# Optimization experiments

Hardware: AMD Instinct MI355X
Metric: run time of the kernel (lower is better)

The kernel has to match this reference:

```python
import jax, jax.numpy as jnp
import numpy as np

HIDDEN = 768
FF = 3072
N_HEADS = 12
HEAD = HIDDEN // N_HEADS
WIDTH = 512  # attention window (number of attended keys, causal)
B, S = 2, 4096
EPS = 1e-6


def _rotary_sincos(seq_len, dim):
    # GPT-J style: freqs per pair, each value repeated twice (interleaved)
    inv_freq = 1.0 / (10000.0 ** (np.arange(0, dim, 2, dtype=np.float32) / dim))
    t = np.arange(seq_len, dtype=np.float32)
    ang = np.einsum('s,d->sd', t, inv_freq)              # [S, dim/2]
    ang = np.repeat(ang, 2, axis=-1)                     # [S, dim]
    return jnp.asarray(np.sin(ang))[:, None, :], jnp.asarray(np.cos(ang))[:, None, :]


def setup_inputs() -> dict:
    key = jax.random.key(0)
    ks = jax.random.split(key, 4)
    x = jax.random.normal(ks[0], (B, S, HIDDEN), dtype=jnp.float32)
    sin, cos = _rotary_sincos(S, HEAD)                   # [S,1,HEAD] each
    W_in = jax.random.normal(ks[1], (HIDDEN, 3 * HIDDEN + FF), dtype=jnp.float32) / np.sqrt(HIDDEN)
    b_in = jnp.zeros((3 * HIDDEN + FF,), dtype=jnp.float32)
    W_out = jax.random.normal(ks[2], (HIDDEN + FF, HIDDEN), dtype=jnp.float32) / np.sqrt(HIDDEN + FF)
    b_out = jnp.zeros((HIDDEN,), dtype=jnp.float32)
    w_norm = jnp.ones((HIDDEN,), dtype=jnp.float32)
    return {"x": x, "sin": sin, "cos": cos, "w_norm": w_norm,
            "W_in": W_in, "b_in": b_in, "W_out": W_out, "b_out": b_out}


def _rotate_every_two(x):
    x1 = x[..., ::2]
    x2 = x[..., 1::2]
    return jnp.stack((-x2, x1), axis=-1).reshape(x.shape)


def _apply_rope(x, sin, cos):
    # x: [B,S,H,hd]; sin/cos: [S,1,hd] -> broadcast as [1,S,1,hd]
    sin = sin[None]
    cos = cos[None]
    return x * cos + _rotate_every_two(x) * sin


def _windowed_attention(q, k, v, width):
    # q,k,v: [B,S,H,hd]; causal local attention: key j valid iff 0 <= i-j < width
    b, s, h, d = q.shape
    wb = width  # block size == window; each query block attends blocks (b-1, b)
    nb = s // wb
    scale = 1.0 / np.sqrt(d)
    qb = q.reshape(b, nb, wb, h, d)
    kp = jnp.pad(k, ((0, 0), (wb, 0), (0, 0), (0, 0))).reshape(b, nb + 1, wb, h, d)
    vp = jnp.pad(v, ((0, 0), (wb, 0), (0, 0), (0, 0))).reshape(b, nb + 1, wb, h, d)
    kb = jnp.concatenate([kp[:, :-1], kp[:, 1:]], axis=2)   # [B,nb,2wb,H,hd]
    vb = jnp.concatenate([vp[:, :-1], vp[:, 1:]], axis=2)
    scores = jnp.einsum('bnqhd,bnkhd->bnhqk', qb, kb) * scale
    qi = jnp.arange(wb)
    ki = jnp.arange(2 * wb)
    bi = jnp.arange(nb)
    diff = wb + qi[:, None] - ki[None, :]                    # i - j per block
    base = (diff >= 0) & (diff < width)                      # [wb, 2wb]
    valid_j = (bi[:, None, None] >= 1) | (ki[None, None, :] >= wb)  # j >= 0
    mask = base[None] & valid_j                              # [nb, wb, 2wb]
    neg = jnp.finfo(scores.dtype).min
    scores = jnp.where(mask[None, :, None], scores, neg)
    p = jax.nn.softmax(scores, axis=-1)
    out = jnp.einsum('bnhqk,bnkhd->bnqhd', p, vb)
    return out.reshape(b, s, h * d)


def reference(x, sin, cos, w_norm, W_in, b_in, W_out, b_out):
    # RMSNorm
    ms = jnp.mean(x * x, axis=-1, keepdims=True)
    xn = x * jax.lax.rsqrt(ms + EPS) * w_norm
    # fused QKV + FF projection
    t = xn @ W_in + b_in                                     # [B,S,3*HIDDEN+FF]
    ff = t[:, :, -FF:]
    qkv = t[:, :, :-FF].reshape(x.shape[0], x.shape[1], 3, N_HEADS, HEAD)
    q = _apply_rope(qkv[:, :, 0], sin, cos)
    k = _apply_rope(qkv[:, :, 1], sin, cos)
    v = qkv[:, :, 2]
    attn = _windowed_attention(q, k, v, WIDTH)               # [B,S,HIDDEN]
    ff = jax.nn.gelu(ff, approximate=False)
    combined = jnp.concatenate((attn, ff), axis=-1)          # [B,S,HIDDEN+FF]
    return combined @ W_out + b_out
```

## Files before the change

kernel.cpp:

```cpp
#include <hip/hip_runtime.h>
#include <hip/hip_bf16.h>

typedef short bf16x8 __attribute__((ext_vector_type(8)));
typedef float f32x4 __attribute__((ext_vector_type(4)));

#define LOG2E 1.4426950408889634f
#define QKV_E ((size_t)24*4096*64)

__device__ __forceinline__ float bfu2f(unsigned short u) {
  unsigned v = ((unsigned)u) << 16;
  return __builtin_bit_cast(float, v);
}
__device__ __forceinline__ unsigned short f2bfu(float f) {
  unsigned u = __builtin_bit_cast(unsigned, f);
  u += 0x7fffu + ((u >> 16) & 1u);
  return (unsigned short)(u >> 16);
}
__device__ __forceinline__ unsigned packbf2(float lo, float hi) {
  return (unsigned)f2bfu(lo) | ((unsigned)f2bfu(hi) << 16);
}
__device__ __forceinline__ float gelu_f(float v) {
  float a = fabsf(v) * 0.70710678118654752f;
  float t = 1.0f / (1.0f + 0.3275911f * a);
  float poly = ((((1.061405429f * t - 1.453152027f) * t + 1.421413741f) * t
                 - 0.284496736f) * t + 0.254829592f) * t;
  float erfa = 1.0f - poly * __expf(-a * a);
  float erfv = v >= 0.0f ? erfa : -erfa;
  return 0.5f * v * (1.0f + erfv);
}
__device__ __forceinline__ void gl_lds16(const ushort* g, ushort* l) {
  __builtin_amdgcn_global_load_lds(
      (const __attribute__((address_space(1))) unsigned int*)(const void*)g,
      (__attribute__((address_space(3))) unsigned int*)(void*)l, 16, 0, 0);
}
#define WAIT_VM8  asm volatile("s_waitcnt vmcnt(8)" ::: "memory")
#define WAIT_VM0  asm volatile("s_waitcnt vmcnt(0)" ::: "memory")
#define WAIT_LGKM asm volatile("s_waitcnt lgkmcnt(0)" ::: "memory")
#define BAR       __builtin_amdgcn_s_barrier()

__global__ __launch_bounds__(256) void rmsnorm_k(const float* __restrict__ x,
    const float* __restrict__ w, ushort* __restrict__ xn) {
  int row = blockIdx.x, t = threadIdx.x;
  const float* xr = x + (size_t)row * 768;
  float v0 = xr[t], v1 = xr[t + 256], v2 = xr[t + 512];
  float ss = v0 * v0 + v1 * v1 + v2 * v2;
#pragma unroll
  for (int m = 32; m >= 1; m >>= 1) ss += __shfl_xor(ss, m, 64);
  __shared__ float part[4];
  if ((t & 63) == 0) part[t >> 6] = ss;
  __syncthreads();
  float tot = part[0] + part[1] + part[2] + part[3];
  float rr = rsqrtf(tot * (1.0f / 768.0f) + 1e-6f);
  ushort* xo = xn + (size_t)row * 768;
  xo[t]       = f2bfu(v0 * rr * w[t]);
  xo[t + 256] = f2bfu(v1 * rr * w[t + 256]);
  xo[t + 512] = f2bfu(v2 * rr * w[t + 512]);
}

__global__ __launch_bounds__(256) void tcvt_k(const float* __restrict__ in,
    ushort* __restrict__ out, int R, int C) {
  __shared__ float tile[32][33];
  int c0 = blockIdx.x * 32, r0 = blockIdx.y * 32;
  int t = threadIdx.x;
  int j = t & 31, i0 = t >> 5;
#pragma unroll
  for (int i = i0; i < 32; i += 8) tile[i][j] = in[(size_t)(r0 + i) * C + c0 + j];
  __syncthreads();
#pragma unroll
  for (int i = i0; i < 32; i += 8) out[(size_t)(c0 + i) * R + r0 + j] = f2bfu(tile[j][i]);
}

__global__ __launch_bounds__(256, 4) void gemm1_k(const ushort* __restrict__ A,
    const ushort* __restrict__ Bt, const float* __restrict__ bias,
    const float* __restrict__ sn, const float* __restrict__ cs,
    ushort* __restrict__ qbuf, ushort* __restrict__ kbuf,
    ushort* __restrict__ vt, ushort* __restrict__ comb) {
  __shared__ __align__(16) ushort lds[2][128 * 64];
  const int t = threadIdx.x, lane = t & 63, w = t >> 6;
  const int wr = w >> 1, wc = w & 1;
  int bid = blockIdx.x;
  int xcd = bid & 7, local = bid >> 3;
  int grp = local / 48, r6 = local % 48;
  int bx = grp * 6 + r6 % 6;
  int by = xcd * 8 + r6 / 6;
  const int mBase = by * 128, nBase = bx * 128;

  size_t gA[4], gB[4];
  int ldst[4];
#pragma unroll
  for (int j = 0; j < 4; ++j) {
    int row = w * 32 + j * 8 + (lane >> 3);
    int gc = ((lane & 7) ^ (lane >> 3)) * 8;
    gA[j] = (size_t)(mBase + row) * 768 + gc;
    gB[j] = (size_t)(nBase + row) * 768 + gc;
    ldst[j] = (w * 32 + j * 8) * 64;
  }

  f32x4 acc[4][4];
  f32x4 z = {0.f, 0.f, 0.f, 0.f};
#pragma unroll
  for (int m = 0; m < 4; ++m)
#pragma unroll
    for (int nn = 0; nn < 4; ++nn) acc[m][nn] = z;

#pragma unroll 1
  for (int kt = 0; kt < 12; ++kt) {
    const int k0 = kt * 64;
    __syncthreads();
#pragma unroll
    for (int j = 0; j < 4; ++j) {
      gl_lds16(A + gA[j] + k0, &lds[0][0] + ldst[j]);
      gl_lds16(Bt + gB[j] + k0, &lds[1][0] + ldst[j]);
    }
    __syncthreads();
#pragma unroll
    for (int kk = 0; kk < 2; ++kk) {
      bf16x8 af[4], bff[4];
#pragma unroll
      for (int m = 0; m < 4; ++m) {
        int row = wr * 64 + m * 16 + (lane & 15);
        int slot = (kk * 4 + (lane >> 4)) ^ (lane & 7);
        af[m] = *(const bf16x8*)(&lds[0][0] + row * 64 + slot * 8);
      }
#pragma unroll
      for (int nn = 0; nn < 4; ++nn) {
        int row = wc * 64 + nn * 16 + (lane & 15);
        int slot = (kk * 4 + (lane >> 4)) ^ (lane & 7);
        bff[nn] = *(const bf16x8*)(&lds[1][0] + row * 64 + slot * 8);
      }
#pragma unroll
      for (int m = 0; m < 4; ++m)
#pragma unroll
        for (int nn = 0; nn < 4; ++nn)
          acc[m][nn] = __builtin_amdgcn_mfma_f32_16x16x32_bf16(bff[nn], af[m], acc[m][nn], 0, 0, 0);
    }
  }

  const bool isff = (nBase >= 2304);
  const int region = nBase / 768;
#pragma unroll
  for (int m = 0; m < 4; ++m) {
    int row = mBase + wr * 64 + m * 16 + (lane & 15);
    int b = row >> 12, s = row & 4095;
#pragma unroll
    for (int nn = 0; nn < 4; ++nn) {
      int col = nBase + wc * 64 + nn * 16 + ((lane >> 4) << 2);
      f32x4 v = acc[m][nn] + *(const f32x4*)(bias + col);
      if (isff) {
        ushort4 o;
        o.x = f2bfu(gelu_f(v[0]));
        o.y = f2bfu(gelu_f(v[1]));
        o.z = f2bfu(gelu_f(v[2]));
        o.w = f2bfu(gelu_f(v[3]));
        *(ushort4*)(comb + (size_t)row * 3840 + (col - 1536)) = o;
      } else {
        int rem = col - region * 768;
        int h = rem >> 6, d0 = rem & 63;
        if (region == 2) {
          int l = s & 127;
          int pnn = l >> 4, pg = (l >> 2) & 3, pr = l & 3;
          int sp = (s & ~127) | (((pnn >> 1) * 4 + pg) * 8 + (pnn & 1) * 4 + pr);
          size_t vb = (size_t)((b * 12 + h) * 64 + d0) * 4096 + sp;
          vt[vb]          = f2bfu(v[0]);
          vt[vb + 4096]   = f2bfu(v[1]);
          vt[vb + 2*4096] = f2bfu(v[2]);
          vt[vb + 3*4096] = f2bfu(v[3]);
        } else {
          f32x4 sv = *(const f32x4*)(sn + (s << 6) + d0);
          f32x4 cv = *(const f32x4*)(cs + (s << 6) + d0);
          float o0 = v[0] * cv[0] - v[1] * sv[0];
          float o1 = v[1] * cv[0] + v[0] * sv[0];
          float o2 = v[2] * cv[2] - v[3] * sv[2];
          float o3 = v[3] * cv[2] + v[2] * sv[2];
          ushort4 o;
          if (region == 0) {
            o.x = f2bfu(o0 * 0.125f); o.y = f2bfu(o1 * 0.125f);
            o.z = f2bfu(o2 * 0.125f); o.w = f2bfu(o3 * 0.125f);
            *(ushort4*)(qbuf + ((size_t)((b * 12 + h) * 4096 + s)) * 64 + d0) = o;
          } else {
            o.x = f2bfu(o0); o.y = f2bfu(o1); o.z = f2bfu(o2); o.w = f2bfu(o3);
            *(ushort4*)(kbuf + ((size_t)((b * 12 + h) * 4096 + s)) * 64 + d0) = o;
          }
        }
      }
    }
  }
}

__global__ __launch_bounds__(256, 4) void gemm2_k(const ushort* __restrict__ A,
    const ushort* __restrict__ Bt, const float* __restrict__ bias,
    float* __restrict__ out) {
  __shared__ __align__(16) ushort lds[2][128 * 64];
  const int t = threadIdx.x, lane = t & 63, w = t >> 6;
  const int wr = w >> 1, wc = w & 1;
  int bid = blockIdx.x;
  int xcd = bid & 7, local = bid >> 3;
  int g = local / 4, r4 = local % 4;
  int bx = (g % 3) * 2 + (r4 & 1);
  int by = xcd * 8 + (g / 3) * 2 + (r4 >> 1);
  const int mBase = by * 128, nBase = bx * 128;

  size_t gA[4], gB[4];
  int ldst[4];
#pragma unroll
  for (int j = 0; j < 4; ++j) {
    int row = w * 32 + j * 8 + (lane >> 3);
    int gc = ((lane & 7) ^ (lane >> 3)) * 8;
    gA[j] = (size_t)(mBase + row) * 3840 + gc;
    gB[j] = (size_t)(nBase + row) * 3840 + gc;
    ldst[j] = (w * 32 + j * 8) * 64;
  }

  f32x4 acc[4][4];
  f32x4 z = {0.f, 0.f, 0.f, 0.f};
#pragma unroll
  for (int m = 0; m < 4; ++m)
#pragma unroll
    for (int nn = 0; nn < 4; ++nn) acc[m][nn] = z;

#pragma unroll 1
  for (int kt = 0; kt < 60; ++kt) {
    const int k0 = kt * 64;
    __syncthreads();
#pragma unroll
    for (int j = 0; j < 4; ++j) {
      gl_lds16(A + gA[j] + k0, &lds[0][0] + ldst[j]);
      gl_lds16(Bt + gB[j] + k0, &lds[1][0] + ldst[j]);
    }
    __syncthreads();
#pragma unroll
    for (int kk = 0; kk < 2; ++kk) {
      bf16x8 af[4], bff[4];
#pragma unroll
      for (int m = 0; m < 4; ++m) {
        int row = wr * 64 + m * 16 + (lane & 15);
        int slot = (kk * 4 + (lane >> 4)) ^ (lane & 7);
        af[m] = *(const bf16x8*)(&lds[0][0] + row * 64 + slot * 8);
      }
#pragma unroll
      for (int nn = 0; nn < 4; ++nn) {
        int row = wc * 64 + nn * 16 + (lane & 15);
        int slot = (kk * 4 + (lane >> 4)) ^ (lane & 7);
        bff[nn] = *(const bf16x8*)(&lds[1][0] + row * 64 + slot * 8);
      }
#pragma unroll
      for (int m = 0; m < 4; ++m)
#pragma unroll
        for (int nn = 0; nn < 4; ++nn)
          acc[m][nn] = __builtin_amdgcn_mfma_f32_16x16x32_bf16(bff[nn], af[m], acc[m][nn], 0, 0, 0);
    }
  }

#pragma unroll
  for (int m = 0; m < 4; ++m) {
    int row = mBase + wr * 64 + m * 16 + (lane & 15);
#pragma unroll
    for (int nn = 0; nn < 4; ++nn) {
      int col = nBase + wc * 64 + nn * 16 + ((lane >> 4) << 2);
      f32x4 v = acc[m][nn] + *(const f32x4*)(bias + col);
      *(f32x4*)(out + (size_t)row * 768 + col) = v;
    }
  }
}

__global__ __launch_bounds__(256, 2) void attn_k(const ushort* __restrict__ qb,
    const ushort* __restrict__ kb, const ushort* __restrict__ vt,
    ushort* __restrict__ comb) {
  __shared__ __align__(16) ushort KS[2][128 * 64];
  __shared__ __align__(16) ushort VS[2][64 * 128];
  int bid = blockIdx.x;
  int nb = (bid & 7) * 96 + (bid >> 3);
  int qt = nb & 31, bh = nb >> 5;
  const int t = threadIdx.x, lane = t & 63, w = t >> 6;
  const int g = lane >> 4, q15 = lane & 15;
  const int qlo = qt * 128;
  const size_t base = (size_t)bh * 4096 * 64;

  size_t kSrc[4], vSrc[4];
  int dstOff[4];
#pragma unroll
  for (int j = 0; j < 4; ++j) {
    int ck = (w * 4 + j) * 64 + lane;
    int key = ck >> 3, sl = ck & 7;
    kSrc[j] = (size_t)key * 64 + ((sl ^ (key & 7)) << 3);
    int dd = ck >> 4, s16 = ck & 15;
    vSrc[j] = (size_t)dd * 4096 + ((s16 ^ (dd & 15)) << 3);
    dstOff[j] = (w * 4 + j) * 512;
  }

  bf16x8 qa[2][2];
#pragma unroll
  for (int m = 0; m < 2; ++m)
#pragma unroll
    for (int kk = 0; kk < 2; ++kk) {
      int row = qlo + w * 32 + m * 16 + q15;
      qa[m][kk] = *(const bf16x8*)(qb + base + (size_t)row * 64 + kk * 32 + g * 8);
    }

  f32x4 z = {0.f, 0.f, 0.f, 0.f};
  f32x4 o[2][4];
#pragma unroll
  for (int m = 0; m < 2; ++m)
#pragma unroll
    for (int df = 0; df < 4; ++df) o[m][df] = z;
  float m_run[2] = {-1e30f, -1e30f}, l_run[2] = {0.f, 0.f};

  const int t0 = qt >= 4 ? qt - 4 : 0;
  const int nt = qt - t0 + 1;
  {
    int k0 = t0 * 128;
#pragma unroll
    for (int j = 0; j < 4; ++j) {
      gl_lds16(kb + base + (size_t)k0 * 64 + kSrc[j], &KS[0][0] + dstOff[j]);
      gl_lds16(vt + base + k0 + vSrc[j], &VS[0][0] + dstOff[j]);
    }
  }

  const int qrow0 = qlo + w * 32 + q15;
#pragma unroll 1
  for (int it = 0; it < nt; ++it) {
    const int kt = t0 + it, k0 = kt * 128, cur = it & 1;
    if (it + 1 < nt) {
      int k1 = k0 + 128;
#pragma unroll
      for (int j = 0; j < 4; ++j) {
        gl_lds16(kb + base + (size_t)k1 * 64 + kSrc[j], &KS[1 - cur][0] + dstOff[j]);
        gl_lds16(vt + base + k1 + vSrc[j], &VS[1 - cur][0] + dstOff[j]);
      }
      WAIT_VM8;
    } else {
      WAIT_VM0;
    }
    BAR;
    f32x4 s[2][8];
#pragma unroll
    for (int m = 0; m < 2; ++m)
#pragma unroll
      for (int nn = 0; nn < 8; ++nn) s[m][nn] = z;
#pragma unroll
    for (int kk = 0; kk < 2; ++kk) {
      bf16x8 kf[8];
#pragma unroll
      for (int nn = 0; nn < 8; ++nn) {
        int row = nn * 16 + q15;
        int slot = (kk * 4 + g) ^ (q15 & 7);
        kf[nn] = *(const bf16x8*)(&KS[cur][0] + row * 64 + slot * 8);
      }
#pragma unroll
      for (int m = 0; m < 2; ++m)
#pragma unroll
        for (int nn = 0; nn < 8; ++nn)
          s[m][nn] = __builtin_amdgcn_mfma_f32_16x16x32_bf16(kf[nn], qa[m][kk], s[m][nn], 0, 0, 0);
    }
    if (kt == qt) {
#pragma unroll
      for (int m = 0; m < 2; ++m) {
        int ql = qrow0 + m * 16 - k0;
#pragma unroll
        for (int nn = 0; nn < 8; ++nn)
#pragma unroll
          for (int r = 0; r < 4; ++r)
            if (nn * 16 + g * 4 + r > ql) s[m][nn][r] = -3e38f;
      }
    } else if (kt == qt - 4) {
#pragma unroll
      for (int m = 0; m < 2; ++m) {
        int ql = qrow0 + m * 16 - k0;
#pragma unroll
        for (int nn = 0; nn < 8; ++nn)
#pragma unroll
          for (int r = 0; r < 4; ++r)
            if (ql - (nn * 16 + g * 4 + r) >= 512) s[m][nn][r] = -3e38f;
      }
    }
    float mx[2];
    bool need = false;
#pragma unroll
    for (int m = 0; m < 2; ++m) {
      float v = s[m][0][0];
#pragma unroll
      for (int nn = 0; nn < 8; ++nn)
#pragma unroll
        for (int r = 0; r < 4; ++r) v = fmaxf(v, s[m][nn][r]);
      v = fmaxf(v, __shfl_xor(v, 16, 64));
      v = fmaxf(v, __shfl_xor(v, 32, 64));
      mx[m] = v;
      need |= (v > m_run[m] + 8.f);
    }
    if (__any(need)) {
#pragma unroll
      for (int m = 0; m < 2; ++m) {
        float mn = fmaxf(m_run[m], mx[m]);
        float sc = exp2f((m_run[m] - mn) * LOG2E);
        m_run[m] = mn;
        l_run[m] *= sc;
#pragma unroll
        for (int df = 0; df < 4; ++df) o[m][df] *= sc;
      }
    }
#pragma unroll
    for (int m = 0; m < 2; ++m) {
      float mr = m_run[m];
      float ls = 0.f;
#pragma unroll
      for (int nn = 0; nn < 8; ++nn)
#pragma unroll
        for (int r = 0; r < 4; ++r) {
          float p = exp2f((s[m][nn][r] - mr) * LOG2E);
          s[m][nn][r] = p;
          ls += p;
        }
      ls += __shfl_xor(ls, 16, 64);
      ls += __shfl_xor(ls, 32, 64);
      l_run[m] += ls;
    }
#pragma unroll
    for (int kk2 = 0; kk2 < 4; ++kk2) {
      bf16x8 pa[2];
#pragma unroll
      for (int m = 0; m < 2; ++m) {
        int4 pi4;
        pi4.x = (int)packbf2(s[m][2*kk2][0],   s[m][2*kk2][1]);
        pi4.y = (int)packbf2(s[m][2*kk2][2],   s[m][2*kk2][3]);
        pi4.z = (int)packbf2(s[m][2*kk2+1][0], s[m][2*kk2+1][1]);
        pi4.w = (int)packbf2(s[m][2*kk2+1][2], s[m][2*kk2+1][3]);
        pa[m] = __builtin_bit_cast(bf16x8, pi4);
      }
#pragma unroll
      for (int df = 0; df < 4; ++df) {
        int row = df * 16 + q15;
        int slot = (kk2 * 4 + g) ^ q15;
        bf16x8 vf = *(const bf16x8*)(&VS[cur][0] + row * 128 + slot * 8);
#pragma unroll
        for (int m = 0; m < 2; ++m)
          o[m][df] = __builtin_amdgcn_mfma_f32_16x16x32_bf16(vf, pa[m], o[m][df], 0, 0, 0);
      }
    }
    WAIT_LGKM;
    BAR;
  }

  int b = bh / 12, h = bh % 12;
#pragma unroll
  for (int m = 0; m < 2; ++m) {
    float inv = 1.0f / l_run[m];
    int row = qrow0 + m * 16;
#pragma unroll
    for (int df = 0; df < 4; ++df) {
      ushort4 ov;
      ov.x = f2bfu(o[m][df][0] * inv);
      ov.y = f2bfu(o[m][df][1] * inv);
      ov.z = f2bfu(o[m][df][2] * inv);
      ov.w = f2bfu(o[m][df][3] * inv);
      *(ushort4*)(comb + (size_t)(b * 4096 + row) * 3840 + h * 64 + df * 16 + g * 4) = ov;
    }
  }
}

extern "C" void kernel_launch(void* const* d_in, const int* in_sizes, int n_in,
                              void* d_out, int out_size, void* d_ws, size_t ws_size,
                              hipStream_t stream) {
  (void)in_sizes; (void)n_in; (void)out_size; (void)ws_size;
  const float* x      = (const float*)d_in[0];
  const float* sin_t  = (const float*)d_in[1];
  const float* cos_t  = (const float*)d_in[2];
  const float* w_norm = (const float*)d_in[3];
  const float* W_in   = (const float*)d_in[4];
  const float* b_in   = (const float*)d_in[5];
  const float* W_out  = (const float*)d_in[6];
  const float* b_out  = (const float*)d_in[7];
  float* out = (float*)d_out;

  const size_t XN_E  = (size_t)8192 * 768;
  ushort* xn      = (ushort*)d_ws;
  ushort* qbuf    = xn + XN_E;
  ushort* kbuf    = qbuf + QKV_E;
  ushort* vt      = kbuf + QKV_E;
  ushort* w_in_t  = vt + QKV_E;
  ushort* w_out_t = w_in_t + (size_t)5376 * 768;
  ushort* comb    = w_out_t + (size_t)768 * 3840;

  rmsnorm_k<<<dim3(8192), dim3(256), 0, stream>>>(x, w_norm, xn);
  tcvt_k<<<dim3(5376 / 32, 768 / 32), dim3(256), 0, stream>>>(W_in, w_in_t, 768, 5376);
  tcvt_k<<<dim3(768 / 32, 3840 / 32), dim3(256), 0, stream>>>(W_out, w_out_t, 3840, 768);
  gemm1_k<<<dim3(2688), dim3(256), 0, stream>>>(xn, w_in_t, b_in, sin_t, cos_t,
                                                qbuf, kbuf, vt, comb);
  attn_k<<<dim3(768), dim3(256), 0, stream>>>(qbuf, kbuf, vt, comb);
  gemm2_k<<<dim3(384), dim3(256), 0, stream>>>(comb, w_out_t, b_out, out);
}
```

Baseline: 231.4 us.

## Split gemm2 K dimension across two warp groups with LDS reduction

The output GEMM now launches 512-thread blocks in which two 256-thread groups each handle half of the K=3840 reduction in their own LDS buffers. The partial accumulators are then summed through LDS in two halves before one group writes the output. With only 384 blocks on a large GPU, this doubles the waves per tile to add parallelism and latency hiding. The cost is doubled LDS per block, extra block-wide barriers that now sync both groups, and a reduction epilogue.

Measured after the change: 224.9 us (median of 2 runs). -2.8%, faster.

```diff
diff --git a/kernel.cpp b/kernel.cpp
--- a/kernel.cpp
+++ b/kernel.cpp
@@ -187,28 +187,31 @@
   }
 }
 
-__global__ __launch_bounds__(256, 4) void gemm2_k(const ushort* __restrict__ A,
+__global__ __launch_bounds__(512, 2) void gemm2_k(const ushort* __restrict__ A,
     const ushort* __restrict__ Bt, const float* __restrict__ bias,
     float* __restrict__ out) {
-  __shared__ __align__(16) ushort lds[2][128 * 64];
-  const int t = threadIdx.x, lane = t & 63, w = t >> 6;
-  const int wr = w >> 1, wc = w & 1;
+  __shared__ __align__(16) ushort lds[2][2][128 * 64];
+  const int t = threadIdx.x;
+  const int grp = t >> 8, tl = t & 255;
+  const int lane = tl & 63, w4 = tl >> 6;
+  const int wr = w4 >> 1, wc = w4 & 1;
   int bid = blockIdx.x;
   int xcd = bid & 7, local = bid >> 3;
   int g = local / 4, r4 = local % 4;
   int bx = (g % 3) * 2 + (r4 & 1);
   int by = xcd * 8 + (g / 3) * 2 + (r4 >> 1);
   const int mBase = by * 128, nBase = bx * 128;
+  const int kOff = grp * 1920;
 
   size_t gA[4], gB[4];
   int ldst[4];
 #pragma unroll
   for (int j = 0; j < 4; ++j) {
-    int row = w * 32 + j * 8 + (lane >> 3);
+    int row = w4 * 32 + j * 8 + (lane >> 3);
     int gc = ((lane & 7) ^ (lane >> 3)) * 8;
-    gA[j] = (size_t)(mBase + row) * 3840 + gc;
-    gB[j] = (size_t)(nBase + row) * 3840 + gc;
-    ldst[j] = (w * 32 + j * 8) * 64;
+    gA[j] = (size_t)(mBase + row) * 3840 + kOff + gc;
+    gB[j] = (size_t)(nBase + row) * 3840 + kOff + gc;
+    ldst[j] = (w4 * 32 + j * 8) * 64;
   }
 
   f32x4 acc[4][4];
@@ -219,13 +222,13 @@
     for (int nn = 0; nn < 4; ++nn) acc[m][nn] = z;
 
 #pragma unroll 1
-  for (int kt = 0; kt < 60; ++kt) {
+  for (int kt = 0; kt < 30; ++kt) {
     const int k0 = kt * 64;
     __syncthreads();
 #pragma unroll
     for (int j = 0; j < 4; ++j) {
-      gl_lds16(A + gA[j] + k0, &lds[0][0] + ldst[j]);
-      gl_lds16(Bt + gB[j] + k0, &lds[1][0] + ldst[j]);
+      gl_lds16(A + gA[j] + k0, &lds[grp][0][0] + ldst[j]);
+      gl_lds16(Bt + gB[j] + k0, &lds[grp][1][0] + ldst[j]);
     }
     __syncthreads();
 #pragma unroll
@@ -235,13 +238,13 @@
       for (int m = 0; m < 4; ++m) {
         int row = wr * 64 + m * 16 + (lane & 15);
         int slot = (kk * 4 + (lane >> 4)) ^ (lane & 7);
-        af[m] = *(const bf16x8*)(&lds[0][0] + row * 64 + slot * 8);
+        af[m] = *(const bf16x8*)(&lds[grp][0][0] + row * 64 + slot * 8);
       }
 #pragma unroll
       for (int nn = 0; nn < 4; ++nn) {
         int row = wc * 64 + nn * 16 + (lane & 15);
         int slot = (kk * 4 + (lane >> 4)) ^ (lane & 7);
-        bff[nn] = *(const bf16x8*)(&lds[1][0] + row * 64 + slot * 8);
+        bff[nn] = *(const bf16x8*)(&lds[grp][1][0] + row * 64 + slot * 8);
       }
 #pragma unroll
       for (int m = 0; m < 4; ++m)
@@ -251,14 +254,30 @@
     }
   }
 
-#pragma unroll
-  for (int m = 0; m < 4; ++m) {
-    int row = mBase + wr * 64 + m * 16 + (lane & 15);
-#pragma unroll
-    for (int nn = 0; nn < 4; ++nn) {
-      int col = nBase + wc * 64 + nn * 16 + ((lane >> 4) << 2);
-      f32x4 v = acc[m][nn] + *(const f32x4*)(bias + col);
-      *(f32x4*)(out + (size_t)row * 768 + col) = v;
+  f32x4* sc = (f32x4*)&lds[0][0][0];
+#pragma unroll
+  for (int h = 0; h < 2; ++h) {
+    __syncthreads();
+    if (grp == 1) {
+#pragma unroll
+      for (int m = 0; m < 2; ++m)
+#pragma unroll
+        for (int nn = 0; nn < 4; ++nn)
+          sc[(size_t)tl * 8 + m * 4 + nn] = acc[2 * h + m][nn];
+    }
+    __syncthreads();
+    if (grp == 0) {
+#pragma unroll
+      for (int m = 0; m < 2; ++m) {
+        int row = mBase + wr * 64 + (2 * h + m) * 16 + (lane & 15);
+#pragma unroll
+        for (int nn = 0; nn < 4; ++nn) {
+          int col = nBase + wc * 64 + nn * 16 + ((lane >> 4) << 2);
+          f32x4 v = acc[2 * h + m][nn] + sc[(size_t)tl * 8 + m * 4 + nn]
+                  + *(const f32x4*)(bias + col);
+          *(f32x4*)(out + (size_t)row * 768 + col) = v;
+        }
+      }
     }
   }
 }
@@ -486,5 +505,5 @@
   gemm1_k<<<dim3(2688), dim3(256), 0, stream>>>(xn, w_in_t, b_in, sin_t, cos_t,
                                                 qbuf, kbuf, vt, comb);
   attn_k<<<dim3(768), dim3(256), 0, stream>>>(qbuf, kbuf, vt, comb);
-  gemm2_k<<<dim3(384), dim3(256), 0, stream>>>(comb, w_out_t, b_out, out);
-}
+  gemm2_k<<<dim3(384), dim3(512), 0, stream>>>(comb, w_out_t, b_out, out);
+}
```
